# Kernel tuning notes

Measured on AMD Instinct MI355X. Metric: run time of the kernel, lower is better.

The kernel has to match this reference:

```python
import jax, jax.numpy as jnp
import numpy as np

RADIUS = 2                 # soft detection radius (init kwarg)
NMS_RADIUS = 2             # hardcoded in detect_keypoints: simple_nms(scores, 2)
TOP_K = 4096
TEMPERATURE = 0.1
KSIZE = 2 * RADIUS + 1     # 5
KK = KSIZE * KSIZE         # 25


def _hw_grid(dtype):
    # flatten order j = dy*KSIZE + dx ; entry = (x_off, y_off)  (torch's [:, [1,0]])
    lin = jnp.linspace(-RADIUS, RADIUS, KSIZE, dtype=dtype)
    gx, gy = jnp.meshgrid(lin, lin)  # 'xy': gx[dy,dx]=lin[dx], gy[dy,dx]=lin[dy]
    return jnp.stack([gx, gy], axis=-1).reshape(-1, 2)  # (KK, 2)


def _maxpool(x, r):
    k = 2 * r + 1
    return jax.lax.reduce_window(x, -jnp.inf, jax.lax.max,
                                 (1, 1, k, k), (1, 1, 1, 1),
                                 ((0, 0), (0, 0), (r, r), (r, r)))


def _simple_nms(scores, r):
    zeros = jnp.zeros_like(scores)
    max_mask = scores == _maxpool(scores, r)
    for _ in range(2):
        supp_mask = _maxpool(max_mask.astype(scores.dtype), r) > 0
        supp_scores = jnp.where(supp_mask, zeros, scores)
        new_max_mask = supp_scores == _maxpool(supp_scores, r)
        max_mask = max_mask | (new_max_mask & ~supp_mask)
    return jnp.where(max_mask, scores, zeros)


def _bilinear_zeros(img, xy):
    # img: (h, w); xy: (K, 2) normalized [-1,1]; align_corners=True, zero padding
    h, w = img.shape
    px = (xy[:, 0] + 1.0) * 0.5 * (w - 1)
    py = (xy[:, 1] + 1.0) * 0.5 * (h - 1)
    x0 = jnp.floor(px); y0 = jnp.floor(py)
    wx1 = px - x0; wx0 = 1.0 - wx1
    wy1 = py - y0; wy0 = 1.0 - wy1
    def tap(xi, yi, wgt):
        valid = (xi >= 0) & (xi < w) & (yi >= 0) & (yi < h)
        xc = jnp.clip(xi, 0, w - 1).astype(jnp.int32)
        yc = jnp.clip(yi, 0, h - 1).astype(jnp.int32)
        return jnp.where(valid, img[yc, xc], 0.0) * wgt
    return (tap(x0, y0, wx0 * wy0) + tap(x0 + 1, y0, wx1 * wy0)
            + tap(x0, y0 + 1, wx0 * wy1) + tap(x0 + 1, y0 + 1, wx1 * wy1))


def _dkd_forward(scores_map):
    b, c, h, w = scores_map.shape
    dtype = scores_map.dtype
    scores_nograd = jax.lax.stop_gradient(scores_map)

    nms_scores = _simple_nms(scores_nograd, NMS_RADIUS)
    # zero out border band of width RADIUS
    ybad = (jnp.arange(h) < RADIUS) | (jnp.arange(h) >= h - RADIUS)
    xbad = (jnp.arange(w) < RADIUS) | (jnp.arange(w) >= w - RADIUS)
    border = ybad[:, None] | xbad[None, :]
    nms_scores = jnp.where(border[None, None], 0.0, nms_scores)

    # top-k over flattened score map (per image)
    _, idx = jax.lax.top_k(nms_scores.reshape(b, -1), TOP_K)  # (b, K)
    ix = idx % w
    iy = idx // w

    # patch gather == unfold(scores_map) + gather, done sparsely with zero pad
    padded = jnp.pad(scores_map[:, 0], ((0, 0), (RADIUS, RADIUS), (RADIUS, RADIUS)))
    off = jnp.arange(KSIZE)
    ys = iy[:, :, None] + off[None, None, :]           # (b, K, KSIZE)
    xs = ix[:, :, None] + off[None, None, :]
    bidx = jnp.arange(b)[:, None, None, None]
    patch_scores = padded[bidx, ys[:, :, :, None], xs[:, :, None, :]]  # (b,K,KSIZE,KSIZE)
    patch_scores = patch_scores.reshape(b, TOP_K, KK)

    hw_grid = _hw_grid(dtype)                          # (KK, 2)
    max_v = jax.lax.stop_gradient(patch_scores.max(axis=-1, keepdims=True))
    x_exp = jnp.exp((patch_scores - max_v) / TEMPERATURE)   # (b,K,KK)
    x_exp_sum = x_exp.sum(axis=-1, keepdims=True)            # (b,K,1)
    xy_residual = jnp.einsum('bkp,pd->bkd', x_exp, hw_grid) / x_exp_sum  # (b,K,2)
    hw_dist2 = (((hw_grid[None, None] - xy_residual[:, :, None]) / RADIUS) ** 2).sum(-1)
    scoredispersity = (x_exp * hw_dist2).sum(-1) / x_exp_sum[..., 0]     # (b,K)

    keypoints_xy_nms = jnp.stack([ix, iy], axis=-1).astype(dtype)
    wh = jnp.array([w - 1, h - 1], dtype=dtype)
    keypoints_xy = (keypoints_xy_nms + xy_residual) / wh * 2.0 - 1.0     # (b,K,2)

    kptscore = jax.vmap(_bilinear_zeros)(scores_map[:, 0], keypoints_xy)  # (b,K)
    return keypoints_xy, kptscore, scoredispersity


def setup_inputs() -> dict:
    key = jax.random.key(0)
    scores_map = jax.random.uniform(key, (8, 1, 1024, 1024), dtype=jnp.float32)
    return {"scores_map": scores_map}


def reference(scores_map):
    # matches torch forward: (keypoints, kptscores, scoredispersitys)
    return _dkd_forward(scores_map)
```

## Files before the change

### kernel.cpp

```cpp
#include <hip/hip_runtime.h>
#include <stdint.h>

namespace {

constexpr int B = 8;
constexpr int H = 1024;
constexpr int W = 1024;
constexpr int TOPK = 4096;
constexpr int CAND_CAP = 131072;
constexpr int SEL_CAP = 16384;
constexpr int LIST_CAP = 320;
constexpr int NHB = 32;

constexpr int RROWS = 78;
constexpr int NG = 20;
constexpr int STR = 80;
constexpr int MW = 5;
constexpr int NSM = 9;
constexpr int NSE = 8;
constexpr int NUNIT_M = NG * NSM;
constexpr int NUNIT_E = NG * NSE;

constexpr int RK_ME = 256;
constexpr int RK_CH = 1024;

constexpr size_t OFF_CNT   = 0;
constexpr size_t OFF_EH    = 4096;
constexpr size_t OFF_FH    = OFF_EH + (size_t)B * 256 * 4;
constexpr size_t OFF_RANK  = OFF_FH + (size_t)B * 256 * 4;
constexpr size_t OFF_SEL   = OFF_RANK + (size_t)B * SEL_CAP * 4;
constexpr size_t OFF_CAND  = OFF_SEL + (size_t)B * SEL_CAP * 8;
constexpr size_t MEMSET_BYTES = OFF_RANK;

__device__ __forceinline__ float max5(float a, float b, float c, float d, float e) {
  return fmaxf(fmaxf(fmaxf(a, b), fmaxf(c, d)), e);
}
__device__ __forceinline__ float4 ld4(const float* p) {
  return *reinterpret_cast<const float4*>(p);
}

template <int PASS>
__device__ __forceinline__ void score_pass(
    int u, int x0, int y0, const float* __restrict__ S,
    const uint32_t* __restrict__ MIN_, uint32_t* __restrict__ MOUT,
    uint64_t* list, uint32_t* cnt_loc, uint64_t* cand, uint32_t* cand_count,
    uint32_t* __restrict__ gehist, int b) {
  const int G = u % NG, s = u / NG;
  const int r0 = ((PASS == 2) ? 8 : 4) + 8 * s;
  const int gx0 = x0 - 8 + 4 * G;
  uint32_t colm = 0;
#pragma unroll
  for (int j = 0; j < 4; ++j)
    if ((unsigned)(gx0 + j) < (unsigned)W) colm |= 1u << j;

  const int p2 = 4 * G - 6;
  const int pw2 = (p2 < 0) ? 0 : (p2 >> 5);
  const int psh2 = (p2 < 0) ? 0 : (p2 & 31);
  const int pls2 = (p2 < 0) ? -p2 : 0;

  float4 hw[5], cw[5];
  uint32_t snr[5], mor[5], cnb[5];
  constexpr int NK = (PASS == 0) ? 12 : 16;
#pragma unroll
  for (int k = 0; k < NK; ++k) {
    if (PASS != 0) {
      const int mr = r0 - 4 + k;
      uint32_t morrow = 0, cnib = 0;
      if ((unsigned)mr < (unsigned)RROWS) {
        const uint32_t* srow = MIN_ + mr * MW;
        uint64_t X = (uint64_t)srow[pw2] | ((uint64_t)srow[pw2 + 1] << 32);
        uint64_t win = pls2 ? (X << pls2) : (X >> psh2);
        uint64_t t5 = win | (win >> 1) | (win >> 2) | (win >> 3) | (win >> 4);
        morrow = (uint32_t)t5 & 0xFFFu;
        cnib = (uint32_t)(win >> 6) & 0xFu;
      }
      mor[k % 5] = morrow;
      cnb[k % 5] = cnib;
    }
    const int ks = (PASS == 0) ? k : k - 4;
    if (ks >= 0) {
      const int sr = r0 - 2 + ks;
      uint32_t supp = 0;
      if (PASS != 0) supp = mor[0] | mor[1] | mor[2] | mor[3] | mor[4];
      const float* rowp = S + sr * STR + 4 * G;
      float4 d = ld4(rowp);
      float4 a = (G > 0) ? ld4(rowp - 4) : d;
      float4 e = (G < NG - 1) ? ld4(rowp + 4) : d;
      if (PASS != 0) {
        if (supp & 0x001u) a.x = 0.f;
        if (supp & 0x002u) a.y = 0.f;
        if (supp & 0x004u) a.z = 0.f;
        if (supp & 0x008u) a.w = 0.f;
        if (supp & 0x010u) d.x = 0.f;
        if (supp & 0x020u) d.y = 0.f;
        if (supp & 0x040u) d.z = 0.f;
        if (supp & 0x080u) d.w = 0.f;
        if (supp & 0x100u) e.x = 0.f;
        if (supp & 0x200u) e.y = 0.f;
        if (supp & 0x400u) e.z = 0.f;
        if (supp & 0x800u) e.w = 0.f;
      }
      float4 hm;
      hm.x = max5(a.z, a.w, d.x, d.y, d.z);
      hm.y = max5(a.w, d.x, d.y, d.z, d.w);
      hm.z = max5(d.x, d.y, d.z, d.w, e.x);
      hm.w = max5(d.y, d.z, d.w, e.x, e.y);
      hw[ks % 5] = hm;
      cw[ks % 5] = d;
      snr[ks % 5] = (supp >> 4) & 0xFu;
      if (ks >= 4) {
        const int rq = r0 - 4 + ks;
        const int gy = y0 - 8 + rq;
        float4 vm;
        vm.x = max5(hw[0].x, hw[1].x, hw[2].x, hw[3].x, hw[4].x);
        vm.y = max5(hw[0].y, hw[1].y, hw[2].y, hw[3].y, hw[4].y);
        vm.z = max5(hw[0].z, hw[1].z, hw[2].z, hw[3].z, hw[4].z);
        vm.w = max5(hw[0].w, hw[1].w, hw[2].w, hw[3].w, hw[4].w);
        float4 c = cw[(ks + 3) % 5];
        uint32_t nm = (uint32_t)(c.x == vm.x) | ((uint32_t)(c.y == vm.y) << 1) |
                      ((uint32_t)(c.z == vm.z) << 2) | ((uint32_t)(c.w == vm.w) << 3);
        nm &= ((unsigned)gy < (unsigned)H) ? colm : 0u;
        const int widx = rq * MW + (G >> 3);
        const int shift = 4 * (G & 7);
        if (PASS == 0) {
          if (nm) atomicOr(&MOUT[widx], nm << shift);
        } else if (PASS == 1) {
          uint32_t fin = cnb[ks % 5] | (nm & ~snr[(ks + 3) % 5]);
          if (fin) atomicOr(&MOUT[widx], fin << shift);
        } else {
          uint32_t fin = cnb[ks % 5] | (nm & ~snr[(ks + 3) % 5]);
          if (fin && G >= 2 && G < 18 && gy >= 2 && gy < H - 2) {
#pragma unroll
            for (int j = 0; j < 4; ++j) {
              if ((fin >> j) & 1u) {
                int gx = gx0 + j;
                if (gx >= 2 && gx < W - 2) {
                  float sval = S[rq * STR + 4 * G + j];
                  if (sval > 0.0f) {
                    uint32_t bits = __float_as_uint(sval);
                    uint32_t flat = (uint32_t)(gy * W + gx);
                    uint64_t key = ((uint64_t)bits << 32) | (uint64_t)(0xFFFFFFFFu - flat);
                    uint32_t pos = atomicAdd(cnt_loc, 1u);
                    if (pos < (uint32_t)LIST_CAP) {
                      list[pos] = key;
                    } else {
                      uint32_t pp = atomicAdd(&cand_count[b], 1u);
                      if (pp < (uint32_t)CAND_CAP) cand[(size_t)b * CAND_CAP + pp] = key;
                      atomicAdd(&gehist[(size_t)b * 256 + (bits >> 23)], 1u);
                    }
                  }
                }
              }
            }
          }
        }
      }
    }
  }
}

__global__ void __launch_bounds__(256, 4) k_nms(const float* __restrict__ scores,
                                                uint64_t* __restrict__ cand,
                                                uint32_t* __restrict__ cand_count,
                                                uint32_t* __restrict__ gehist) {
  __shared__ float S[RROWS * STR];
  __shared__ uint32_t M0s[RROWS * MW];
  __shared__ uint32_t M1s[RROWS * MW];
  __shared__ uint64_t list[LIST_CAP];
  __shared__ uint32_t cnt_loc, base_g;
  const int b = blockIdx.z;
  const int x0 = blockIdx.x * 64, y0 = blockIdx.y * 64;
  const int tid = threadIdx.x;
  const float* img = scores + (size_t)b * H * W;
  if (tid == 0) cnt_loc = 0;

  for (int u = tid; u < RROWS * NG; u += 256) {
    int r = u / NG, G = u % NG;
    int gy = y0 - 8 + r, gx = x0 - 8 + 4 * G;
    float4 v;
    if ((unsigned)gy < (unsigned)H && (unsigned)gx < (unsigned)W)
      v = ld4(img + (size_t)gy * W + gx);
    else
      v = make_float4(-INFINITY, -INFINITY, -INFINITY, -INFINITY);
    *reinterpret_cast<float4*>(&S[r * STR + 4 * G]) = v;
  }
  for (int i = tid; i < RROWS * MW; i += 256) {
    M0s[i] = 0;
    M1s[i] = 0;
  }
  __syncthreads();
  if (tid < NUNIT_M)
    score_pass<0>(tid, x0, y0, S, nullptr, M0s, nullptr, nullptr, nullptr, nullptr,
                  nullptr, b);
  __syncthreads();
  if (tid < NUNIT_M)
    score_pass<1>(tid, x0, y0, S, M0s, M1s, nullptr, nullptr, nullptr, nullptr,
                  nullptr, b);
  __syncthreads();
  if (tid < NUNIT_E)
    score_pass<2>(tid, x0, y0, S, M1s, nullptr, list, &cnt_loc, cand, cand_count,
                  gehist, b);
  __syncthreads();
  uint32_t nblk = cnt_loc;
  uint32_t nmain = nblk < (uint32_t)LIST_CAP ? nblk : (uint32_t)LIST_CAP;
  if (tid == 0) base_g = atomicAdd(&cand_count[b], nmain);
  M0s[tid] = 0;
  __syncthreads();
  uint32_t bg = base_g;
  for (uint32_t i = tid; i < nmain; i += 256) {
    uint64_t key = list[i];
    uint32_t pp = bg + i;
    if (pp < (uint32_t)CAND_CAP) cand[(size_t)b * CAND_CAP + pp] = key;
    atomicAdd(&M0s[(uint32_t)(key >> 55)], 1u);
  }
  __syncthreads();
  uint32_t v = M0s[tid];
  if (v) atomicAdd(&gehist[(size_t)b * 256 + tid], v);
}

__global__ void __launch_bounds__(256) k_fhist(const uint64_t* __restrict__ cand,
                                               const uint32_t* __restrict__ cand_count,
                                               const uint32_t* __restrict__ gehist,
                                               uint32_t* __restrict__ gfhist) {
  __shared__ uint32_t fh[256];
  __shared__ uint32_t ehl[256];
  __shared__ int sE;
  const int b = blockIdx.y, t = threadIdx.x;
  uint32_t n = cand_count[b];
  if (n > (uint32_t)CAND_CAP) n = CAND_CAP;
  fh[t] = 0;
  ehl[t] = gehist[b * 256 + t];
  __syncthreads();
  if (t == 0) {
    uint32_t run = 0;
    int E = -1;
    for (int e = 255; e >= 0; --e) {
      uint32_t nrun = run + ehl[e];
      if (run < (uint32_t)TOPK && nrun >= (uint32_t)TOPK) E = e;
      run = nrun;
    }
    if (run < (uint32_t)TOPK) E = -1;
    sE = E;
  }
  __syncthreads();
  const int E = sE;
  if (E < 0) return;
  const uint64_t* cb = cand + (size_t)b * CAND_CAP;
  for (uint32_t i = blockIdx.x * 256 + t; i < n; i += NHB * 256) {
    uint64_t key = cb[i];
    if ((uint32_t)(key >> 55) == (uint32_t)E)
      atomicAdd(&fh[(uint32_t)(key >> 47) & 0xFFu], 1u);
  }
  __syncthreads();
  uint32_t v = fh[t];
  if (v) atomicAdd(&gfhist[b * 256 + t], v);
}

__global__ void __launch_bounds__(1024) k_compact(const uint64_t* __restrict__ cand,
                                                  const uint32_t* __restrict__ cand_count,
                                                  const uint32_t* __restrict__ gehist,
                                                  const uint32_t* __restrict__ gfhist,
                                                  uint64_t* __restrict__ sel,
                                                  uint32_t* __restrict__ sel_count,
                                                  uint32_t* __restrict__ rankg) {
  __shared__ uint64_t list[1024];
  __shared__ uint32_t cnt_loc, base_g;
  __shared__ uint32_t eh[256], fh[256];
  __shared__ int sE;
  __shared__ uint32_t sAbove;
  __shared__ uint64_t s_thr;
  const int b = blockIdx.y;
  uint32_t n = cand_count[b];
  if (n > (uint32_t)CAND_CAP) n = CAND_CAP;
  const int tid = threadIdx.x;
  if (tid == 0) {
    cnt_loc = 0;
    sE = -1;
    s_thr = 0ull;
  }
  if (tid < 256) {
    eh[tid] = gehist[b * 256 + tid];
    fh[tid] = gfhist[b * 256 + tid];
  }
  __syncthreads();
  for (int d = 1; d < 256; d <<= 1) {
    uint32_t ve = 0, vf = 0;
    if (tid < 256) {
      ve = (tid + d < 256) ? eh[tid + d] : 0u;
      vf = (tid + d < 256) ? fh[tid + d] : 0u;
    }
    __syncthreads();
    if (tid < 256) {
      eh[tid] += ve;
      fh[tid] += vf;
    }
    __syncthreads();
  }
  if (tid < 256) {
    uint32_t nxt = (tid < 255) ? eh[tid + 1] : 0u;
    if (eh[tid] >= (uint32_t)TOPK && nxt < (uint32_t)TOPK) {
      sE = tid;
      sAbove = nxt;
    }
  }
  __syncthreads();
  if (sE >= 0 && tid < 256) {
    uint32_t above = sAbove;
    uint32_t Fn = (tid < 255) ? fh[tid + 1] : 0u;
    if (above + fh[tid] >= (uint32_t)TOPK && above + Fn < (uint32_t)TOPK)
      s_thr = ((uint64_t)(((uint32_t)sE << 8) | (uint32_t)tid)) << 47;
  }
  __syncthreads();
  const uint64_t thr = s_thr;
  uint32_t i = blockIdx.x * 1024 + tid;
  if (i < n) {
    uint64_t key = cand[(size_t)b * CAND_CAP + i];
    if (key >= thr) {
      uint32_t pos = atomicAdd(&cnt_loc, 1u);
      list[pos] = key;
    }
  }
  __syncthreads();
  uint32_t nblk = cnt_loc;
  if (tid == 0 && nblk > 0) base_g = atomicAdd(&sel_count[b], nblk);
  __syncthreads();
  if (nblk > 0 && (uint32_t)tid < nblk) {
    uint32_t pp = base_g + tid;
    if (pp < (uint32_t)SEL_CAP) {
      sel[(size_t)b * SEL_CAP + pp] = list[tid];
      rankg[(size_t)b * SEL_CAP + pp] = 0u;
    }
  }
}

__global__ void __launch_bounds__(RK_ME) k_rank_part(const uint64_t* __restrict__ sel,
                                                     const uint32_t* __restrict__ sel_count,
                                                     uint32_t* __restrict__ rankg) {
  __shared__ uint64_t keys[RK_CH];
  const int b = blockIdx.z;
  uint32_t n = sel_count[b];
  if (n > (uint32_t)SEL_CAP) n = SEL_CAP;
  const uint32_t me0 = blockIdx.x * RK_ME;
  const uint32_t c0 = blockIdx.y * RK_CH;
  if (me0 >= n || c0 >= n) return;
  const uint64_t* sb = sel + (size_t)b * SEL_CAP;
  uint32_t clen = n - c0;
  if (clen > (uint32_t)RK_CH) clen = RK_CH;
  for (uint32_t i = threadIdx.x; i < clen; i += RK_ME) keys[i] = sb[c0 + i];
  __syncthreads();
  const uint32_t me = me0 + threadIdx.x;
  if (me >= n) return;
  const uint64_t kme = sb[me];
  uint32_t rank = 0;
  uint32_t i = 0;
  for (; i + 8 <= clen; i += 8) {
    rank += (keys[i] > kme);
    rank += (keys[i + 1] > kme);
    rank += (keys[i + 2] > kme);
    rank += (keys[i + 3] > kme);
    rank += (keys[i + 4] > kme);
    rank += (keys[i + 5] > kme);
    rank += (keys[i + 6] > kme);
    rank += (keys[i + 7] > kme);
  }
  for (; i < clen; ++i) rank += (keys[i] > kme);
  if (rank) atomicAdd(&rankg[(size_t)b * SEL_CAP + me], rank);
}

__global__ void __launch_bounds__(256) k_refine(const float* __restrict__ scores,
                                                const uint64_t* __restrict__ sel,
                                                const uint32_t* __restrict__ sel_count,
                                                const uint32_t* __restrict__ rankg,
                                                float* __restrict__ out) {
  int gid = blockIdx.x * 256 + threadIdx.x;
  int idx = gid >> 3, ln = gid & 7;
  const int b = idx / SEL_CAP;
  const int i = idx % SEL_CAP;
  uint32_t n = sel_count[b];
  if (n > (uint32_t)SEL_CAP) n = SEL_CAP;
  if ((uint32_t)i >= n) return;
  uint32_t r = rankg[(size_t)b * SEL_CAP + i];
  if (r >= (uint32_t)TOPK) return;
  uint64_t key = sel[(size_t)b * SEL_CAP + i];
  uint32_t flat = 0xFFFFFFFFu - (uint32_t)(key & 0xFFFFFFFFull);
  if (flat >= (uint32_t)(H * W)) flat = 0;
  const int ix = (int)(flat % W);
  const int iy = (int)(flat / W);
  const float* img = scores + (size_t)b * H * W;

  const int nt = (ln == 0) ? 4 : 3;
  float v[4];
  float mymax = -INFINITY;
#pragma unroll
  for (int q = 0; q < 4; ++q) {
    if (q < nt) {
      int t = ln + 8 * q;
      int y = iy + t / 5 - 2, x = ix + t % 5 - 2;
      float val = ((unsigned)x < (unsigned)W && (unsigned)y < (unsigned)H)
                      ? img[(size_t)y * W + x] : 0.0f;
      v[q] = val;
      mymax = fmaxf(mymax, val);
    }
  }
#pragma unroll
  for (int m = 1; m < 8; m <<= 1) mymax = fmaxf(mymax, __shfl_xor(mymax, m));
  float e[4];
  float sum = 0.f, sx = 0.f, sy = 0.f;
#pragma unroll
  for (int q = 0; q < 4; ++q) {
    if (q < nt) {
      int t = ln + 8 * q;
      float ev = expf((v[q] - mymax) / 0.1f);
      e[q] = ev;
      sum += ev;
      sx += ev * (float)(t % 5 - 2);
      sy += ev * (float)(t / 5 - 2);
    }
  }
#pragma unroll
  for (int m = 1; m < 8; m <<= 1) {
    sum += __shfl_xor(sum, m);
    sx += __shfl_xor(sx, m);
    sy += __shfl_xor(sy, m);
  }
  float rx = sx / sum, ry = sy / sum;
  float dsp = 0.f;
#pragma unroll
  for (int q = 0; q < 4; ++q) {
    if (q < nt) {
      int t = ln + 8 * q;
      float dx = ((float)(t % 5 - 2) - rx) * 0.5f;
      float dy = ((float)(t / 5 - 2) - ry) * 0.5f;
      dsp += e[q] * (dx * dx + dy * dy);
    }
  }
#pragma unroll
  for (int m = 1; m < 8; m <<= 1) dsp += __shfl_xor(dsp, m);
  if (ln != 0) return;
  dsp /= sum;
  float kx = ((float)ix + rx) / 1023.0f * 2.0f - 1.0f;
  float ky = ((float)iy + ry) / 1023.0f * 2.0f - 1.0f;
  float px = (kx + 1.0f) * 0.5f * 1023.0f;
  float py = (ky + 1.0f) * 0.5f * 1023.0f;
  float x0f = floorf(px), y0f = floorf(py);
  float wx1 = px - x0f, wx0 = 1.0f - wx1;
  float wy1 = py - y0f, wy0 = 1.0f - wy1;
  int x0 = (int)x0f, y0 = (int)y0f;
  float sc = 0.0f;
  {
    int xs[2] = {x0, x0 + 1};
    int ys[2] = {y0, y0 + 1};
    float wxs[2] = {wx0, wx1};
    float wys[2] = {wy0, wy1};
#pragma unroll
    for (int yy = 0; yy < 2; ++yy)
#pragma unroll
      for (int xx = 0; xx < 2; ++xx) {
        int xi = xs[xx], yi = ys[yy];
        bool valid = (xi >= 0 && xi < W && yi >= 0 && yi < H);
        int xc = min(max(xi, 0), W - 1);
        int yc = min(max(yi, 0), H - 1);
        float vv = valid ? img[(size_t)yc * W + xc] : 0.0f;
        sc += vv * (wxs[xx] * wys[yy]);
      }
  }
  out[((size_t)b * TOPK + r) * 2 + 0] = kx;
  out[((size_t)b * TOPK + r) * 2 + 1] = ky;
  out[(size_t)B * TOPK * 2 + (size_t)b * TOPK + r] = sc;
  out[(size_t)B * TOPK * 3 + (size_t)b * TOPK + r] = dsp;
}

}

extern "C" void kernel_launch(void* const* d_in, const int* in_sizes, int n_in,
                              void* d_out, int out_size, void* d_ws, size_t ws_size,
                              hipStream_t stream) {
  const float* scores = (const float*)d_in[0];
  float* out = (float*)d_out;
  char* ws = (char*)d_ws;

  uint32_t* cnt = (uint32_t*)(ws + OFF_CNT);
  uint32_t* cand_count = cnt;
  uint32_t* sel_count  = cnt + 8;
  uint32_t* gehist = (uint32_t*)(ws + OFF_EH);
  uint32_t* gfhist = (uint32_t*)(ws + OFF_FH);
  uint32_t* rankg = (uint32_t*)(ws + OFF_RANK);
  uint64_t* sel  = (uint64_t*)(ws + OFF_SEL);
  uint64_t* cand = (uint64_t*)(ws + OFF_CAND);

  hipMemsetAsync(ws + OFF_CNT, 0, MEMSET_BYTES, stream);

  k_nms<<<dim3(W / 64, H / 64, B), 256, 0, stream>>>(scores, cand, cand_count, gehist);
  k_fhist<<<dim3(NHB, B), 256, 0, stream>>>(cand, cand_count, gehist, gfhist);
  k_compact<<<dim3(CAND_CAP / 1024, B), 1024, 0, stream>>>(cand, cand_count, gehist,
                                                           gfhist, sel, sel_count, rankg);
  k_rank_part<<<dim3(SEL_CAP / RK_ME, SEL_CAP / RK_CH, B), RK_ME, 0, stream>>>(
      sel, sel_count, rankg);
  k_refine<<<(B * SEL_CAP * 8) / 256, 256, 0, stream>>>(scores, sel, sel_count, rankg,
                                                        out);
}
```

Measured before the change: 195.5 us.

## Replace two-level radix histogram with single fine histogram built during NMS

The exponent histogram plus a separate refinement-histogram kernel is replaced by one 3840-bin histogram over the top 15 bits of the float key, accumulated in shared memory inside the NMS kernel. The compaction kernel scans the fine histogram directly to find the top-K threshold, and blocks past the candidate count now exit early. This removes the k_fhist launch and its second pass over the candidate array. In exchange, NMS blocks do more shared-memory zeroing and flush more global atomics, and values below the histogram base are clamped into bin 0, which assumes scores lie in a known range.

Result: faster. 188.0 us (-3.8%).

```diff
diff --git a/kernel.cpp b/kernel.cpp
--- a/kernel.cpp
+++ b/kernel.cpp
@@ -10,7 +10,9 @@
 constexpr int CAND_CAP = 131072;
 constexpr int SEL_CAP = 16384;
 constexpr int LIST_CAP = 320;
-constexpr int NHB = 32;
+
+constexpr int HIST_BINS = 3840;
+constexpr int HIST_BASE = 112 << 8;
 
 constexpr int RROWS = 78;
 constexpr int NG = 20;
@@ -25,9 +27,8 @@
 constexpr int RK_CH = 1024;
 
 constexpr size_t OFF_CNT   = 0;
-constexpr size_t OFF_EH    = 4096;
-constexpr size_t OFF_FH    = OFF_EH + (size_t)B * 256 * 4;
-constexpr size_t OFF_RANK  = OFF_FH + (size_t)B * 256 * 4;
+constexpr size_t OFF_GH    = 4096;
+constexpr size_t OFF_RANK  = OFF_GH + (size_t)B * HIST_BINS * 4;
 constexpr size_t OFF_SEL   = OFF_RANK + (size_t)B * SEL_CAP * 4;
 constexpr size_t OFF_CAND  = OFF_SEL + (size_t)B * SEL_CAP * 8;
 constexpr size_t MEMSET_BYTES = OFF_RANK;
@@ -44,7 +45,7 @@
     int u, int x0, int y0, const float* __restrict__ S,
     const uint32_t* __restrict__ MIN_, uint32_t* __restrict__ MOUT,
     uint64_t* list, uint32_t* cnt_loc, uint64_t* cand, uint32_t* cand_count,
-    uint32_t* __restrict__ gehist, int b) {
+    uint32_t* __restrict__ ghist, int b) {
   const int G = u % NG, s = u / NG;
   const int r0 = ((PASS == 2) ? 8 : 4) + 8 * s;
   const int gx0 = x0 - 8 + 4 * G;
@@ -146,7 +147,10 @@
                     } else {
                       uint32_t pp = atomicAdd(&cand_count[b], 1u);
                       if (pp < (uint32_t)CAND_CAP) cand[(size_t)b * CAND_CAP + pp] = key;
-                      atomicAdd(&gehist[(size_t)b * 256 + (bits >> 23)], 1u);
+                      int bin = (int)(bits >> 15) - HIST_BASE;
+                      if (bin < 0) bin = 0;
+                      if (bin >= HIST_BINS) bin = HIST_BINS - 1;
+                      atomicAdd(&ghist[(size_t)b * HIST_BINS + bin], 1u);
                     }
                   }
                 }
@@ -162,7 +166,7 @@
 __global__ void __launch_bounds__(256, 4) k_nms(const float* __restrict__ scores,
                                                 uint64_t* __restrict__ cand,
                                                 uint32_t* __restrict__ cand_count,
-                                                uint32_t* __restrict__ gehist) {
+                                                uint32_t* __restrict__ ghist) {
   __shared__ float S[RROWS * STR];
   __shared__ uint32_t M0s[RROWS * MW];
   __shared__ uint32_t M1s[RROWS * MW];
@@ -199,116 +203,82 @@
   __syncthreads();
   if (tid < NUNIT_E)
     score_pass<2>(tid, x0, y0, S, M1s, nullptr, list, &cnt_loc, cand, cand_count,
-                  gehist, b);
+                  ghist, b);
   __syncthreads();
   uint32_t nblk = cnt_loc;
   uint32_t nmain = nblk < (uint32_t)LIST_CAP ? nblk : (uint32_t)LIST_CAP;
   if (tid == 0) base_g = atomicAdd(&cand_count[b], nmain);
-  M0s[tid] = 0;
+  uint32_t* Shist = (uint32_t*)S;
+  for (int i = tid; i < HIST_BINS; i += 256) Shist[i] = 0;
   __syncthreads();
   uint32_t bg = base_g;
   for (uint32_t i = tid; i < nmain; i += 256) {
     uint64_t key = list[i];
     uint32_t pp = bg + i;
     if (pp < (uint32_t)CAND_CAP) cand[(size_t)b * CAND_CAP + pp] = key;
-    atomicAdd(&M0s[(uint32_t)(key >> 55)], 1u);
-  }
-  __syncthreads();
-  uint32_t v = M0s[tid];
-  if (v) atomicAdd(&gehist[(size_t)b * 256 + tid], v);
-}
-
-__global__ void __launch_bounds__(256) k_fhist(const uint64_t* __restrict__ cand,
-                                               const uint32_t* __restrict__ cand_count,
-                                               const uint32_t* __restrict__ gehist,
-                                               uint32_t* __restrict__ gfhist) {
-  __shared__ uint32_t fh[256];
-  __shared__ uint32_t ehl[256];
-  __shared__ int sE;
-  const int b = blockIdx.y, t = threadIdx.x;
-  uint32_t n = cand_count[b];
-  if (n > (uint32_t)CAND_CAP) n = CAND_CAP;
-  fh[t] = 0;
-  ehl[t] = gehist[b * 256 + t];
-  __syncthreads();
-  if (t == 0) {
-    uint32_t run = 0;
-    int E = -1;
-    for (int e = 255; e >= 0; --e) {
-      uint32_t nrun = run + ehl[e];
-      if (run < (uint32_t)TOPK && nrun >= (uint32_t)TOPK) E = e;
-      run = nrun;
-    }
-    if (run < (uint32_t)TOPK) E = -1;
-    sE = E;
-  }
-  __syncthreads();
-  const int E = sE;
-  if (E < 0) return;
-  const uint64_t* cb = cand + (size_t)b * CAND_CAP;
-  for (uint32_t i = blockIdx.x * 256 + t; i < n; i += NHB * 256) {
-    uint64_t key = cb[i];
-    if ((uint32_t)(key >> 55) == (uint32_t)E)
-      atomicAdd(&fh[(uint32_t)(key >> 47) & 0xFFu], 1u);
-  }
-  __syncthreads();
-  uint32_t v = fh[t];
-  if (v) atomicAdd(&gfhist[b * 256 + t], v);
+    int bin = (int)(uint32_t)(key >> 47) - HIST_BASE;
+    if (bin < 0) bin = 0;
+    atomicAdd(&Shist[bin], 1u);
+  }
+  __syncthreads();
+  for (int i = tid; i < HIST_BINS; i += 256) {
+    uint32_t v = Shist[i];
+    if (v) atomicAdd(&ghist[(size_t)b * HIST_BINS + i], v);
+  }
 }
 
 __global__ void __launch_bounds__(1024) k_compact(const uint64_t* __restrict__ cand,
                                                   const uint32_t* __restrict__ cand_count,
-                                                  const uint32_t* __restrict__ gehist,
-                                                  const uint32_t* __restrict__ gfhist,
+                                                  const uint32_t* __restrict__ ghist,
                                                   uint64_t* __restrict__ sel,
                                                   uint32_t* __restrict__ sel_count,
                                                   uint32_t* __restrict__ rankg) {
   __shared__ uint64_t list[1024];
   __shared__ uint32_t cnt_loc, base_g;
-  __shared__ uint32_t eh[256], fh[256];
-  __shared__ int sE;
-  __shared__ uint32_t sAbove;
+  __shared__ uint32_t h[1024];
   __shared__ uint64_t s_thr;
   const int b = blockIdx.y;
   uint32_t n = cand_count[b];
   if (n > (uint32_t)CAND_CAP) n = CAND_CAP;
+  if (blockIdx.x * 1024u >= n) return;
   const int tid = threadIdx.x;
   if (tid == 0) {
     cnt_loc = 0;
-    sE = -1;
     s_thr = 0ull;
   }
-  if (tid < 256) {
-    eh[tid] = gehist[b * 256 + tid];
-    fh[tid] = gfhist[b * 256 + tid];
-  }
-  __syncthreads();
-  for (int d = 1; d < 256; d <<= 1) {
-    uint32_t ve = 0, vf = 0;
-    if (tid < 256) {
-      ve = (tid + d < 256) ? eh[tid + d] : 0u;
-      vf = (tid + d < 256) ? fh[tid + d] : 0u;
-    }
+  const uint32_t* gh = ghist + (size_t)b * HIST_BINS;
+  uint4 mybins = make_uint4(0u, 0u, 0u, 0u);
+  uint32_t s = 0;
+  if (tid < HIST_BINS / 4) {
+    mybins = reinterpret_cast<const uint4*>(gh)[tid];
+    s = mybins.x + mybins.y + mybins.z + mybins.w;
+  }
+  h[tid] = s;
+  __syncthreads();
+  for (int d = 1; d < 1024; d <<= 1) {
+    uint32_t v = (tid + d < 1024) ? h[tid + d] : 0u;
     __syncthreads();
-    if (tid < 256) {
-      eh[tid] += ve;
-      fh[tid] += vf;
-    }
+    h[tid] += v;
     __syncthreads();
   }
-  if (tid < 256) {
-    uint32_t nxt = (tid < 255) ? eh[tid + 1] : 0u;
-    if (eh[tid] >= (uint32_t)TOPK && nxt < (uint32_t)TOPK) {
-      sE = tid;
-      sAbove = nxt;
-    }
-  }
-  __syncthreads();
-  if (sE >= 0 && tid < 256) {
-    uint32_t above = sAbove;
-    uint32_t Fn = (tid < 255) ? fh[tid + 1] : 0u;
-    if (above + fh[tid] >= (uint32_t)TOPK && above + Fn < (uint32_t)TOPK)
-      s_thr = ((uint64_t)(((uint32_t)sE << 8) | (uint32_t)tid)) << 47;
+  {
+    uint32_t cum = h[tid];
+    uint32_t nxt = (tid < 1023) ? h[tid + 1] : 0u;
+    if (cum >= (uint32_t)TOPK && nxt < (uint32_t)TOPK) {
+      uint32_t run = nxt;
+      uint32_t binv[4] = {mybins.x, mybins.y, mybins.z, mybins.w};
+      int thrbin = 4 * tid;
+#pragma unroll
+      for (int j = 3; j >= 0; --j) {
+        run += binv[j];
+        if (run >= (uint32_t)TOPK) {
+          thrbin = 4 * tid + j;
+          break;
+        }
+      }
+      if (thrbin > 0)
+        s_thr = ((uint64_t)(uint32_t)(thrbin + HIST_BASE)) << 47;
+    }
   }
   __syncthreads();
   const uint64_t thr = s_thr;
@@ -482,18 +452,16 @@
   uint32_t* cnt = (uint32_t*)(ws + OFF_CNT);
   uint32_t* cand_count = cnt;
   uint32_t* sel_count  = cnt + 8;
-  uint32_t* gehist = (uint32_t*)(ws + OFF_EH);
-  uint32_t* gfhist = (uint32_t*)(ws + OFF_FH);
+  uint32_t* ghist = (uint32_t*)(ws + OFF_GH);
   uint32_t* rankg = (uint32_t*)(ws + OFF_RANK);
   uint64_t* sel  = (uint64_t*)(ws + OFF_SEL);
   uint64_t* cand = (uint64_t*)(ws + OFF_CAND);
 
   hipMemsetAsync(ws + OFF_CNT, 0, MEMSET_BYTES, stream);
 
-  k_nms<<<dim3(W / 64, H / 64, B), 256, 0, stream>>>(scores, cand, cand_count, gehist);
-  k_fhist<<<dim3(NHB, B), 256, 0, stream>>>(cand, cand_count, gehist, gfhist);
-  k_compact<<<dim3(CAND_CAP / 1024, B), 1024, 0, stream>>>(cand, cand_count, gehist,
-                                                           gfhist, sel, sel_count, rankg);
+  k_nms<<<dim3(W / 64, H / 64, B), 256, 0, stream>>>(scores, cand, cand_count, ghist);
+  k_compact<<<dim3(CAND_CAP / 1024, B), 1024, 0, stream>>>(cand, cand_count, ghist,
+                                                           sel, sel_count, rankg);
   k_rank_part<<<dim3(SEL_CAP / RK_ME, SEL_CAP / RK_CH, B), RK_ME, 0, stream>>>(
       sel, sel_count, rankg);
   k_refine<<<(B * SEL_CAP * 8) / 256, 256, 0, stream>>>(scores, sel, sel_count, rankg,
```
